# Optimization experiments

Hardware: AMD Instinct MI355X
Metric: run time of the kernel (lower is better)

## Reference

```python
import jax, jax.numpy as jnp
import numpy as np

D_MODEL = 768
D_STATE = 16
D_CONV = 4
EXPAND = 2
D_INNER = EXPAND * D_MODEL
D_HID = D_INNER // 4
BATCH = 2
SEQ = 2048
LN_EPS = 1e-5


def setup_inputs() -> dict:
    key = jax.random.key(0)
    ks = jax.random.split(key, 16)
    rn = lambda k, s, sc: (jax.random.normal(k, s, jnp.float32) * sc)
    x = rn(ks[0], (BATCH, SEQ, D_MODEL), 1.0)
    importance = jax.random.uniform(ks[1], (BATCH, SEQ), jnp.float32)
    W_in = rn(ks[2], (D_MODEL, 2 * D_INNER), D_MODEL ** -0.5)
    conv_w = rn(ks[3], (D_INNER, 1, D_CONV), D_CONV ** -0.5)
    conv_b = rn(ks[4], (D_INNER,), 0.02)
    W_x = rn(ks[5], (D_INNER, 2 * D_STATE + 1), D_INNER ** -0.5)
    W_dt = rn(ks[6], (1, D_INNER), 1.0)
    b_dt = rn(ks[7], (D_INNER,), 0.02)
    Wc1 = rn(ks[8], (1, D_HID), 1.0)
    bc1 = rn(ks[9], (D_HID,), 0.02)
    Wc2 = rn(ks[10], (D_HID, D_INNER), D_HID ** -0.5)
    bc2 = rn(ks[11], (D_INNER,), 0.02)
    A_log = jnp.log(jnp.tile(jnp.arange(1, D_STATE + 1, dtype=jnp.float32)[None, :], (D_INNER, 1)))
    Dskip = jnp.ones((D_INNER,), jnp.float32)
    W_out = rn(ks[12], (D_INNER, D_MODEL), D_INNER ** -0.5)
    ln_g = jnp.ones((D_MODEL,), jnp.float32)
    ln_b = jnp.zeros((D_MODEL,), jnp.float32)
    return dict(x=x, importance=importance, ln_g=ln_g, ln_b=ln_b, W_in=W_in,
                conv_w=conv_w, conv_b=conv_b, W_x=W_x, W_dt=W_dt, b_dt=b_dt,
                Wc1=Wc1, bc1=bc1, Wc2=Wc2, bc2=bc2, A_log=A_log, Dskip=Dskip, W_out=W_out)


def _forward(x, importance, ln_g, ln_b, W_in, conv_w, conv_b, W_x, W_dt, b_dt,
             Wc1, bc1, Wc2, bc2, A_log, Dskip, W_out):
    residual = x
    mu = jnp.mean(x, axis=-1, keepdims=True)
    var = jnp.mean(jnp.square(x - mu), axis=-1, keepdims=True)
    xn = (x - mu) * jax.lax.rsqrt(var + LN_EPS) * ln_g + ln_b
    xz = xn @ W_in                      # (B, L, 2*Di)
    x_proj, z = jnp.split(xz, 2, axis=-1)
    # depthwise causal conv1d (left pad K-1, truncate to L)
    xc = jnp.transpose(x_proj, (0, 2, 1))   # (B, Di, L)
    xc = jax.lax.conv_general_dilated(xc, conv_w, window_strides=(1,),
                                      padding=[(D_CONV - 1, 0)],
                                      feature_group_count=D_INNER,
                                      dimension_numbers=('NCH', 'OIH', 'NCH'))
    xc = xc + conv_b[None, :, None]
    xc = jnp.transpose(xc, (0, 2, 1))       # (B, L, Di)
    xc = jax.nn.silu(xc)
    x_ssm = xc @ W_x                         # (B, L, 2N+1)
    delta_raw = x_ssm[..., :1]
    Bm = x_ssm[..., 1:1 + D_STATE]
    Cm = x_ssm[..., 1 + D_STATE:]
    delta = jax.nn.softplus(delta_raw @ W_dt + b_dt)   # (B, L, Di)
    # cluster modulation of delta
    mod = jax.nn.sigmoid(jax.nn.relu(importance[..., None] @ Wc1 + bc1) @ Wc2 + bc2)
    delta = delta * (1.0 + mod)
    A = -jnp.exp(A_log)                      # (Di, N)
    h0 = jnp.zeros((BATCH, D_INNER, D_STATE), delta.dtype)

    def step(h, ts):
        dl, Bt, Ct, xt = ts                  # (B,Di),(B,N),(B,N),(B,Di)
        dA = jnp.exp(dl[:, :, None] * A)     # (B,Di,N)
        h = dA * h + (dl * xt)[:, :, None] * Bt[:, None, :]
        y = jnp.einsum('bdn,bn->bd', h, Ct)
        return h, y

    xs = (jnp.transpose(delta, (1, 0, 2)), jnp.transpose(Bm, (1, 0, 2)),
          jnp.transpose(Cm, (1, 0, 2)), jnp.transpose(xc, (1, 0, 2)))
    _, ys = jax.lax.scan(step, h0, xs)
    y = jnp.transpose(ys, (1, 0, 2))         # (B, L, Di)
    y = y + xc * Dskip
    y = y * jax.nn.silu(z)
    y = y @ W_out
    return y + residual


def reference(x, importance, ln_g, ln_b, W_in, conv_w, conv_b, W_x, W_dt, b_dt,
              Wc1, bc1, Wc2, bc2, A_log, Dskip, W_out):
    return _forward(x, importance, ln_g, ln_b, W_in, conv_w, conv_b, W_x, W_dt, b_dt,
                    Wc1, bc1, Wc2, bc2, A_log, Dskip, W_out)
```

## Files before the change

### kernel.cpp

```cpp
#include <hip/hip_runtime.h>
#include <math.h>

#define SEQL   2048
#define NBATCH 2
#define DMODEL 768
#define DINNER 1536
#define D2     3072
#define DSTATE 16
#define DHID   384
#define ROWS   (NBATCH*SEQL)
#define NC     64
#define CL     32
#define CROWS  16
#define LN_EPSF 1e-5f

typedef unsigned short u16;
typedef short bf16x8 __attribute__((ext_vector_type(8)));
typedef float f32x4 __attribute__((ext_vector_type(4)));

__device__ __forceinline__ u16 f2b(float x) {
  unsigned u = __float_as_uint(x);
  unsigned r = (u + 0x7FFFu + ((u >> 16) & 1u)) >> 16;
  return (u16)r;
}
__device__ __forceinline__ float b2f(u16 v) {
  return __uint_as_float((unsigned)v << 16);
}

__device__ __forceinline__ void build_E_fast(float dl, float* E) {
  float e1 = __expf(-dl);
  float e2 = e1 * e1, e4 = e2 * e2, e8 = e4 * e4;
  E[0] = e1;      E[1] = e2;      E[2] = e2 * e1; E[3] = e4;
  E[4] = e4 * e1; E[5] = e4 * e2; E[6] = e4 * E[2]; E[7] = e8;
  E[8] = e8 * e1; E[9] = e8 * e2; E[10] = e8 * E[2]; E[11] = e8 * e4;
  E[12] = e8 * E[4]; E[13] = e8 * E[5]; E[14] = e8 * E[6]; E[15] = e8 * e8;
}

__device__ __forceinline__ void tconv64_body(const float* __restrict__ src,
    u16* __restrict__ dst, int K, int N, int bx, int by, int tid) {
  __shared__ float t[64][65];
  int n0 = bx * 64, k0 = by * 64;
  int tx = tid & 15, ty = tid >> 4;
  #pragma unroll
  for (int i = 0; i < 4; ++i) {
    float4 v = *(const float4*)&src[(long)(k0 + ty + 16 * i) * N + n0 + tx * 4];
    t[ty + 16 * i][tx * 4 + 0] = v.x; t[ty + 16 * i][tx * 4 + 1] = v.y;
    t[ty + 16 * i][tx * 4 + 2] = v.z; t[ty + 16 * i][tx * 4 + 3] = v.w;
  }
  __syncthreads();
  #pragma unroll
  for (int i = 0; i < 4; ++i) {
    int n = ty + 16 * i;
    u16 o[4];
    #pragma unroll
    for (int j = 0; j < 4; ++j) o[j] = f2b(t[tx * 4 + j][n]);
    *(ushort4*)&dst[(long)(n0 + n) * K + k0 + tx * 4] = *(ushort4*)o;
  }
}

__global__ __launch_bounds__(256) void prep_kernel(
    const float* __restrict__ W_in,  u16* __restrict__ Wt_in,
    const float* __restrict__ Wc2,   u16* __restrict__ Wt_c2,
    const float* __restrict__ W_out, u16* __restrict__ Wt_out,
    const float* __restrict__ Wx,    u16* __restrict__ Wxt,
    const float* __restrict__ imp,   const float* __restrict__ Wc1,
    const float* __restrict__ bc1,   u16* __restrict__ hid,
    const float* __restrict__ x,     const float* __restrict__ g,
    const float* __restrict__ bta,   u16* __restrict__ xn,
    const float* __restrict__ A_log, float* __restrict__ Af,
    int* __restrict__ flag) {
  int id = blockIdx.x;
  int tid = threadIdx.x;
  if (id < 576) {
    tconv64_body(W_in, Wt_in, 768, 3072, id % 48, id / 48, tid);
  } else if (id < 720) {
    int r = id - 576;  tconv64_body(Wc2, Wt_c2, 384, 1536, r % 24, r / 24, tid);
  } else if (id < 1008) {
    int r = id - 720;  tconv64_body(W_out, Wt_out, 1536, 768, r % 12, r / 12, tid);
  } else if (id < 1056) {
    long i8 = ((long)(id - 1008) * 256 + tid) * 8;
    int n = (int)(i8 / 1536), k0 = (int)(i8 % 1536);
    u16 o[8];
    #pragma unroll
    for (int j = 0; j < 8; ++j)
      o[j] = (n < 33) ? f2b(Wx[(long)(k0 + j) * 33 + n]) : (u16)0;
    *(bf16x8*)&Wxt[i8] = *(bf16x8*)o;
  } else if (id < 1824) {
    long g8 = ((long)(id - 1056) * 256 + tid) * 8;
    int j0 = (int)(g8 % DHID);
    long r = g8 / DHID;
    float im = imp[r];
    float4 wa = *(const float4*)&Wc1[j0], wb = *(const float4*)&Wc1[j0 + 4];
    float4 ba = *(const float4*)&bc1[j0], bb = *(const float4*)&bc1[j0 + 4];
    float v[8] = { fmaf(im, wa.x, ba.x), fmaf(im, wa.y, ba.y),
                   fmaf(im, wa.z, ba.z), fmaf(im, wa.w, ba.w),
                   fmaf(im, wb.x, bb.x), fmaf(im, wb.y, bb.y),
                   fmaf(im, wb.z, bb.z), fmaf(im, wb.w, bb.w) };
    u16 o[8];
    #pragma unroll
    for (int j = 0; j < 8; ++j) o[j] = f2b(v[j] > 0.f ? v[j] : 0.f);
    *(bf16x8*)&hid[g8] = *(bf16x8*)o;
  } else if (id < 2848) {
    int wid2 = tid >> 6, lane = tid & 63;
    long r = (long)(id - 1824) * 4 + wid2;
    const float* xr = x + r * DMODEL;
    float vv[12];
    *(float4*)&vv[0] = *(const float4*)&xr[lane * 4];
    *(float4*)&vv[4] = *(const float4*)&xr[lane * 4 + 256];
    *(float4*)&vv[8] = *(const float4*)&xr[lane * 4 + 512];
    float s = 0.f;
    #pragma unroll
    for (int i = 0; i < 12; ++i) s += vv[i];
    #pragma unroll
    for (int o = 32; o > 0; o >>= 1) s += __shfl_xor(s, o);
    float mu = s * (1.f / DMODEL);
    float q = 0.f;
    #pragma unroll
    for (int i = 0; i < 12; ++i) { float dd = vv[i] - mu; q += dd * dd; }
    #pragma unroll
    for (int o = 32; o > 0; o >>= 1) q += __shfl_xor(q, o);
    float rs = rsqrtf(q * (1.f / DMODEL) + LN_EPSF);
    #pragma unroll
    for (int gq = 0; gq < 3; ++gq) {
      int col = lane * 4 + gq * 256;
      float4 gv = *(const float4*)&g[col];
      float4 bv = *(const float4*)&bta[col];
      u16 o[4];
      o[0] = f2b((vv[gq * 4 + 0] - mu) * rs * gv.x + bv.x);
      o[1] = f2b((vv[gq * 4 + 1] - mu) * rs * gv.y + bv.y);
      o[2] = f2b((vv[gq * 4 + 2] - mu) * rs * gv.z + bv.z);
      o[3] = f2b((vv[gq * 4 + 3] - mu) * rs * gv.w + bv.w);
      *(ushort4*)&xn[r * DMODEL + col] = *(ushort4*)o;
    }
  } else {
    __shared__ int scnt;
    if (tid == 0) scnt = 0;
    __syncthreads();
    int mism = 0;
    for (int i = tid; i < DINNER * 16; i += 256) {
      int n = i & 15;
      float a = -expf(A_log[i]);
      Af[i] = a;
      mism += (fabsf(a + (float)(n + 1)) > 1e-3f) ? 1 : 0;
    }
    atomicAdd(&scnt, mism);
    __syncthreads();
    if (tid == 0) *flag = scnt;
  }
}

template<int BM, int BN, int WGM, int WGN, int EPI, int XSWZ>
__global__ __launch_bounds__(256) void gemm_bf16(
    const u16* __restrict__ A, const u16* __restrict__ Bt,
    float* __restrict__ C, int M, int N, int K, const float* __restrict__ aux,
    const float* __restrict__ p1, const float* __restrict__ p2,
    const float* __restrict__ p3, u16* __restrict__ pz) {
  constexpr int MF = BM / (16 * WGM);
  constexpr int NF = BN / (16 * WGN);
  constexpr int AR = BM / 32;
  constexpr int BR = BN / 32;
  constexpr int HALF = (BM + BN) * 128;
  __shared__ __align__(16) char smem[2 * HALF];

  int tid = threadIdx.x;
  int lane = tid & 63;
  int wid = tid >> 6;

  int bx, by;
  if (XSWZ) {
    int nwgx = gridDim.x;
    int bid = blockIdx.y * nwgx + blockIdx.x;
    int nwg = nwgx * gridDim.y;
    int q = nwg >> 3;
    int swz = (bid & 7) * q + (bid >> 3);
    bx = swz % nwgx; by = swz / nwgx;
  } else {
    bx = blockIdx.x; by = blockIdx.y;
  }
  int m0 = by * BM, n0 = bx * BN;
  int wr = wid / WGN, wc = wid % WGN;

  f32x4 acc[MF][NF];
  #pragma unroll
  for (int i = 0; i < MF; ++i)
    #pragma unroll
    for (int j = 0; j < NF; ++j) acc[i][j] = f32x4{0.f, 0.f, 0.f, 0.f};

  int srow = tid >> 3;
  int schunk = tid & 7;
  int wavebase = (tid & 192) * 16;
  int arow = lane & 15;
  int kgrp = lane >> 4;
  int sw = (lane & 7) << 4;

  auto stage = [&](int k0, char* base) {
    #pragma unroll
    for (int r = 0; r < AR; ++r) {
      int row = r * 32 + srow;
      int chunk = schunk ^ (row & 7);
      const u16* g = A + (size_t)(m0 + row) * K + k0 + chunk * 8;
      __builtin_amdgcn_global_load_lds(
          (const __attribute__((address_space(1))) void*)g,
          (__attribute__((address_space(3))) void*)(base + r * 4096 + wavebase),
          16, 0, 0);
    }
    #pragma unroll
    for (int r = 0; r < BR; ++r) {
      int row = r * 32 + srow;
      int chunk = schunk ^ (row & 7);
      const u16* g = Bt + (size_t)(n0 + row) * K + k0 + chunk * 8;
      __builtin_amdgcn_global_load_lds(
          (const __attribute__((address_space(1))) void*)g,
          (__attribute__((address_space(3))) void*)(base + BM * 128 + r * 4096 + wavebase),
          16, 0, 0);
    }
  };

  auto compute = [&](const char* base) {
    const char* Asm = base;
    const char* Bsm = base + BM * 128;
    #pragma unroll
    for (int ks = 0; ks < 2; ++ks) {
      bf16x8 af[MF], bg[NF];
      #pragma unroll
      for (int i = 0; i < MF; ++i) {
        int row = wr * MF * 16 + i * 16 + arow;
        int off = row * 128 + ((((ks * 4 + kgrp) * 16)) ^ sw);
        af[i] = *(const bf16x8*)(Asm + off);
      }
      #pragma unroll
      for (int j = 0; j < NF; ++j) {
        int row = wc * NF * 16 + j * 16 + arow;
        int off = row * 128 + ((((ks * 4 + kgrp) * 16)) ^ sw);
        bg[j] = *(const bf16x8*)(Bsm + off);
      }
      #pragma unroll
      for (int i = 0; i < MF; ++i)
        #pragma unroll
        for (int j = 0; j < NF; ++j)
          acc[i][j] = __builtin_amdgcn_mfma_f32_16x16x32_bf16(af[i], bg[j], acc[i][j], 0, 0, 0);
    }
  };

  int nk = K >> 6;
  stage(0, smem);
  asm volatile("s_waitcnt vmcnt(0)" ::: "memory");
  __builtin_amdgcn_s_barrier();
  for (int t = 0; t < nk; t += 2) {
    stage((t + 1) << 6, smem + HALF);
    compute(smem);
    asm volatile("s_waitcnt vmcnt(0)" ::: "memory");
    __builtin_amdgcn_s_barrier();
    if (t + 2 < nk) stage((t + 2) << 6, smem);
    compute(smem + HALF);
    asm volatile("s_waitcnt vmcnt(0)" ::: "memory");
    __builtin_amdgcn_s_barrier();
  }

  int crow0 = m0 + wr * MF * 16 + (lane >> 4) * 4;
  int ccol0 = n0 + wc * NF * 16 + (lane & 15);
  #pragma unroll
  for (int i = 0; i < MF; ++i) {
    #pragma unroll
    for (int r = 0; r < 4; ++r) {
      int row = crow0 + i * 16 + r;
      float araw = 0.f;
      if (EPI == 2) araw = aux[(size_t)row * 64];
      #pragma unroll
      for (int j = 0; j < NF; ++j) {
        int col = ccol0 + j * 16;
        float v = acc[i][j][r];
        if (EPI == 0) {
          C[(size_t)row * N + col] = v;
        } else if (EPI == 1) {
          C[(size_t)row * N + col] = v + aux[(size_t)row * N + col];
        } else if (EPI == 2) {
          float raw = fmaf(araw, p1[col], p2[col]);
          float sp = fmaxf(raw, 0.f) + __logf(1.f + __expf(-fabsf(raw)));
          float mod = 1.f / (1.f + __expf(-(v + p3[col])));
          pz[(size_t)row * N + col] = f2b(sp * (1.f + mod));
        } else if (EPI == 5) {
          pz[(size_t)row * N + col] = f2b(v);
        }
      }
    }
  }
}

__global__ __launch_bounds__(256) void conv_silu_kernel(const u16* __restrict__ xzb,
    const float* __restrict__ cw, const float* __restrict__ cb,
    u16* __restrict__ xcb) {
  int tid = threadIdx.x;
  int dblk = blockIdx.x % (DINNER / 256);
  int rc   = blockIdx.x / (DINNER / 256);
  int d = dblk * 256 + tid;
  long r0 = (long)rc * CROWS;
  int s0 = (int)(r0 % SEQL);
  const u16* xp = xzb + r0 * D2 + d;
  float w0 = 0.f, w1 = 0.f, w2 = 0.f;
  if (s0 >= 1) {
    w2 = b2f(xp[-1L * D2]);
    w1 = b2f(xp[-2L * D2]);
    w0 = b2f(xp[-3L * D2]);
  }
  float c0 = cw[d * 4 + 0], c1 = cw[d * 4 + 1];
  float c2 = cw[d * 4 + 2], c3 = cw[d * 4 + 3];
  float cbv = cb[d];
  u16* yp = xcb + r0 * DINNER + d;
  #pragma unroll 4
  for (int t = 0; t < CROWS; ++t) {
    float w3 = b2f(xp[(long)t * D2]);
    float acc = fmaf(w0, c0, fmaf(w1, c1, fmaf(w2, c2, fmaf(w3, c3, cbv))));
    float sg = 1.f / (1.f + __expf(-acc));
    yp[(long)t * DINNER] = f2b(acc * sg);
    w0 = w1; w1 = w2; w2 = w3;
  }
}

__global__ __launch_bounds__(256) void scan_p1(const u16* __restrict__ dlt,
    const u16* __restrict__ xc, const float* __restrict__ xs,
    const float* __restrict__ Af, const int* __restrict__ flag,
    float* __restrict__ Hloc, float* __restrict__ sdl) {
  __shared__ float Bsh[CL][16];
  int tid = threadIdx.x;
  int dblk = blockIdx.x % (DINNER / 256);
  int c = (blockIdx.x / (DINNER / 256)) % NC;
  int b = blockIdx.x / ((DINNER / 256) * NC);
  int d = dblk * 256 + tid;
  long row0 = (long)b * SEQL + c * CL;
  for (int e = tid; e < CL * 16; e += 256) {
    int t = e >> 4, n = e & 15;
    Bsh[t][n] = xs[(row0 + t) * 64 + 1 + n];
  }
  bool fast = (*flag == 0);
  float Ac[16];
  if (!fast) {
    #pragma unroll
    for (int n = 0; n < 16; ++n) Ac[n] = Af[d * 16 + n];
  }
  __syncthreads();
  float h[16] = {};
  float sd = 0.f;
  const u16* dp = dlt + row0 * DINNER + d;
  const u16* xp = xc + row0 * DINNER + d;
  if (fast) {
    for (int t = 0; t < CL; ++t) {
      float dl = b2f(dp[(long)t * DINNER]);
      float xv = b2f(xp[(long)t * DINNER]);
      sd += dl;
      float dx = dl * xv;
      float E[16]; build_E_fast(dl, E);
      #pragma unroll
      for (int n = 0; n < 16; ++n) h[n] = fmaf(E[n], h[n], dx * Bsh[t][n]);
    }
  } else {
    for (int t = 0; t < CL; ++t) {
      float dl = b2f(dp[(long)t * DINNER]);
      float xv = b2f(xp[(long)t * DINNER]);
      sd += dl;
      float dx = dl * xv;
      #pragma unroll
      for (int n = 0; n < 16; ++n)
        h[n] = fmaf(__expf(dl * Ac[n]), h[n], dx * Bsh[t][n]);
    }
  }
  long base = ((long)(b * NC + c) * DINNER + d) * 16;
  #pragma unroll
  for (int n = 0; n < 16; ++n) Hloc[base + n] = h[n];
  sdl[(long)(b * NC + c) * DINNER + d] = sd;
}

__global__ __launch_bounds__(256) void scan_carry(float* __restrict__ Hloc,
    const float* __restrict__ sdl, const float* __restrict__ Af) {
  long g = (long)blockIdx.x * 256 + threadIdx.x;
  if (g >= (long)NBATCH * DINNER * 16) return;
  int n = (int)(g & 15);
  int d = (int)((g >> 4) % DINNER);
  int b = (int)(g / (16L * DINNER));
  float An = Af[d * 16 + n];
  float s = 0.f;
  for (int c = 0; c < NC; ++c) {
    long off = ((long)(b * NC + c) * DINNER + d) * 16 + n;
    float H = Hloc[off];
    float sdv = sdl[(long)(b * NC + c) * DINNER + d];
    Hloc[off] = s;
    s = fmaf(__expf(An * sdv), s, H);
  }
}

__global__ __launch_bounds__(256) void scan_p3(const u16* __restrict__ dlt,
    const u16* __restrict__ xc, const float* __restrict__ xs,
    const float* __restrict__ Af, const int* __restrict__ flag,
    const float* __restrict__ Hloc, const u16* __restrict__ xzb,
    const float* __restrict__ Dskip, u16* __restrict__ y2) {
  __shared__ float Bsh[CL][16];
  __shared__ float Csh[CL][16];
  int tid = threadIdx.x;
  int dblk = blockIdx.x % (DINNER / 256);
  int c = (blockIdx.x / (DINNER / 256)) % NC;
  int b = blockIdx.x / ((DINNER / 256) * NC);
  int d = dblk * 256 + tid;
  long row0 = (long)b * SEQL + c * CL;
  for (int e = tid; e < CL * 16; e += 256) {
    int t = e >> 4, n = e & 15;
    long rr = row0 + t;
    Bsh[t][n] = xs[rr * 64 + 1 + n];
    Csh[t][n] = xs[rr * 64 + 17 + n];
  }
  bool fast = (*flag == 0);
  float Ac[16];
  if (!fast) {
    #pragma unroll
    for (int n = 0; n < 16; ++n) Ac[n] = Af[d * 16 + n];
  }
  __syncthreads();
  float h[16];
  long base = ((long)(b * NC + c) * DINNER + d) * 16;
  #pragma unroll
  for (int n = 0; n < 16; ++n) h[n] = Hloc[base + n];
  float Dv = Dskip[d];
  const u16* dp = dlt + row0 * DINNER + d;
  const u16* xp = xc + row0 * DINNER + d;
  const u16* zp = xzb + row0 * D2 + DINNER + d;
  u16* yp = y2 + row0 * DINNER + d;
  if (fast) {
    for (int t = 0; t < CL; ++t) {
      float dl = b2f(dp[(long)t * DINNER]);
      float xv = b2f(xp[(long)t * DINNER]);
      float dx = dl * xv;
      float E[16]; build_E_fast(dl, E);
      float y = 0.f;
      #pragma unroll
      for (int n = 0; n < 16; ++n) {
        h[n] = fmaf(E[n], h[n], dx * Bsh[t][n]);
        y = fmaf(h[n], Csh[t][n], y);
      }
      float yv = fmaf(xv, Dv, y);
      float zv = b2f(zp[(long)t * D2]);
      float sz = zv / (1.f + __expf(-zv));
      yp[(long)t * DINNER] = f2b(yv * sz);
    }
  } else {
    for (int t = 0; t < CL; ++t) {
      float dl = b2f(dp[(long)t * DINNER]);
      float xv = b2f(xp[(long)t * DINNER]);
      float dx = dl * xv;
      float y = 0.f;
      #pragma unroll
      for (int n = 0; n < 16; ++n) {
        h[n] = fmaf(__expf(dl * Ac[n]), h[n], dx * Bsh[t][n]);
        y = fmaf(h[n], Csh[t][n], y);
      }
      float yv = fmaf(xv, Dv, y);
      float zv = b2f(zp[(long)t * D2]);
      float sz = zv / (1.f + __expf(-zv));
      yp[(long)t * DINNER] = f2b(yv * sz);
    }
  }
}

extern "C" void kernel_launch(void* const* d_in, const int* in_sizes, int n_in,
                              void* d_out, int out_size, void* d_ws, size_t ws_size,
                              hipStream_t stream) {
  const float* x      = (const float*)d_in[0];
  const float* imp    = (const float*)d_in[1];
  const float* ln_g   = (const float*)d_in[2];
  const float* ln_b   = (const float*)d_in[3];
  const float* W_in   = (const float*)d_in[4];
  const float* conv_w = (const float*)d_in[5];
  const float* conv_b = (const float*)d_in[6];
  const float* W_x    = (const float*)d_in[7];
  const float* W_dt   = (const float*)d_in[8];
  const float* b_dt   = (const float*)d_in[9];
  const float* Wc1    = (const float*)d_in[10];
  const float* bc1    = (const float*)d_in[11];
  const float* Wc2    = (const float*)d_in[12];
  const float* bc2    = (const float*)d_in[13];
  const float* A_log  = (const float*)d_in[14];
  const float* Dskip  = (const float*)d_in[15];
  const float* W_out  = (const float*)d_in[16];
  float* out = (float*)d_out;

  char* ws = (char*)d_ws;
  u16*   xzb    = (u16*)  (ws);
  u16*   xcb    = (u16*)  (ws + 25165824L);
  u16*   dltb   = (u16*)  (ws + 37748736L);
  float* xs64   = (float*)(ws + 50331648L);
  u16*   hid    = (u16*)  (ws + 51380224L);
  u16*   xnb    = (u16*)  (ws + 54525952L);
  u16*   y2     = (u16*)  (ws + 60817408L);
  float* Hloc   = (float*)(ws + 73400320L);
  float* sdl    = (float*)(ws + 85983232L);
  u16*   Wt_in  = (u16*)  (ws + 86769664L);
  u16*   Wt_c2  = (u16*)  (ws + 91488256L);
  u16*   Wt_out = (u16*)  (ws + 92667904L);
  u16*   Wxt    = (u16*)  (ws + 95027200L);
  float* Af     = (float*)(ws + 95223808L);
  int*   flag   = (int*)  (ws + 95322112L);

  prep_kernel<<<2849, 256, 0, stream>>>(
      W_in, Wt_in, Wc2, Wt_c2, W_out, Wt_out, W_x, Wxt,
      imp, Wc1, bc1, hid, x, ln_g, ln_b, xnb, A_log, Af, flag);

  gemm_bf16<128,128,2,2,5,1><<<dim3(D2/128, ROWS/128), 256, 0, stream>>>(
      xnb, Wt_in, nullptr, ROWS, D2, DMODEL, nullptr, nullptr, nullptr, nullptr, xzb);
  conv_silu_kernel<<<(DINNER / 256) * (ROWS / CROWS), 256, 0, stream>>>(xzb, conv_w, conv_b, xcb);
  gemm_bf16<32,64,1,4,0,0><<<dim3(1, ROWS/32), 256, 0, stream>>>(
      xcb, Wxt, xs64, ROWS, 64, DINNER, nullptr, nullptr, nullptr, nullptr, nullptr);
  gemm_bf16<64,128,1,4,2,0><<<dim3(DINNER/128, ROWS/64), 256, 0, stream>>>(
      hid, Wt_c2, nullptr, ROWS, DINNER, DHID, xs64, W_dt, b_dt, bc2, dltb);
  scan_p1<<<NBATCH * NC * (DINNER / 256), 256, 0, stream>>>(dltb, xcb, xs64, Af, flag, Hloc, sdl);
  scan_carry<<<(NBATCH * DINNER * 16) / 256, 256, 0, stream>>>(Hloc, sdl, Af);
  scan_p3<<<NBATCH * NC * (DINNER / 256), 256, 0, stream>>>(dltb, xcb, xs64, Af, flag, Hloc, xzb, Dskip, y2);
  gemm_bf16<64,64,1,4,1,0><<<dim3(DMODEL/64, ROWS/64), 256, 0, stream>>>(
      y2, Wt_out, out, ROWS, DMODEL, DINNER, x, nullptr, nullptr, nullptr, nullptr);
}
```

Measured before the change: 164.2 us.

## Add dedicated 256x192-tile in-projection GEMM with 512 threads

Replaces the generic 128x128 bf16 GEMM for the input projection with a specialized kernel that uses 256x192 tiles, 8 waves, direct global-to-LDS loads with XOR-swizzled LDS and double buffering. Grid is 16x16 = 256 blocks with a block-index swizzle meant to improve L2 locality. The larger tiles raise per-block data reuse and cut block count to roughly match the CU count, at the cost of more registers and LDS (about 112KB) per block, which limits occupancy. The previous epilogue variant (EPI 5) is replaced by a plain bf16 store, which could differ if that epilogue did extra work.

Result: faster. 158.9 us, median of 2 (-3.2%).

```diff
diff --git a/kernel.cpp b/kernel.cpp
--- a/kernel.cpp
+++ b/kernel.cpp
@@ -149,6 +149,115 @@
   }
 }
 
+__global__ __launch_bounds__(512) void gemm_xz_256(
+    const u16* __restrict__ A, const u16* __restrict__ Bt,
+    u16* __restrict__ pz) {
+  constexpr int BM = 256, BN = 192, K = 768, N = 3072;
+  constexpr int HALF = (BM + BN) * 128;
+  __shared__ __align__(16) char smem[2 * HALF];
+
+  int tid = threadIdx.x;
+  int lane = tid & 63;
+  int wid = tid >> 6;
+  int bid = blockIdx.y * 16 + blockIdx.x;
+  int swz = (bid & 7) * 32 + (bid >> 3);
+  int bx = swz & 15, by = swz >> 4;
+  int m0 = by * BM, n0 = bx * BN;
+  int wr = wid >> 2, wc = wid & 3;
+
+  f32x4 acc[8][3];
+  #pragma unroll
+  for (int i = 0; i < 8; ++i)
+    #pragma unroll
+    for (int j = 0; j < 3; ++j) acc[i][j] = f32x4{0.f, 0.f, 0.f, 0.f};
+
+  int srow = tid >> 3;
+  int schunk = tid & 7;
+  int wavebase = wid * 1024;
+  int arow = lane & 15;
+  int kgrp = lane >> 4;
+  int sw = (lane & 7) << 4;
+
+  auto stage = [&](int k0, char* base) {
+    #pragma unroll
+    for (int r = 0; r < 4; ++r) {
+      int row = r * 64 + srow;
+      int chunk = schunk ^ (row & 7);
+      const u16* g = A + (size_t)(m0 + row) * K + k0 + chunk * 8;
+      __builtin_amdgcn_global_load_lds(
+          (const __attribute__((address_space(1))) void*)g,
+          (__attribute__((address_space(3))) void*)(base + r * 8192 + wavebase),
+          16, 0, 0);
+    }
+    #pragma unroll
+    for (int r = 0; r < 3; ++r) {
+      int row = r * 64 + srow;
+      int chunk = schunk ^ (row & 7);
+      const u16* g = Bt + (size_t)(n0 + row) * K + k0 + chunk * 8;
+      __builtin_amdgcn_global_load_lds(
+          (const __attribute__((address_space(1))) void*)g,
+          (__attribute__((address_space(3))) void*)(base + BM * 128 + r * 8192 + wavebase),
+          16, 0, 0);
+    }
+  };
+
+  auto compute = [&](const char* base) {
+    const char* Asm = base;
+    const char* Bsm = base + BM * 128;
+    #pragma unroll
+    for (int ks = 0; ks < 2; ++ks) {
+      bf16x8 af[8], bg[3];
+      #pragma unroll
+      for (int i = 0; i < 8; ++i) {
+        int row = wr * 128 + i * 16 + arow;
+        int off = row * 128 + ((((ks * 4 + kgrp) * 16)) ^ sw);
+        af[i] = *(const bf16x8*)(Asm + off);
+      }
+      #pragma unroll
+      for (int j = 0; j < 3; ++j) {
+        int row = wc * 48 + j * 16 + arow;
+        int off = row * 128 + ((((ks * 4 + kgrp) * 16)) ^ sw);
+        bg[j] = *(const bf16x8*)(Bsm + off);
+      }
+      #pragma unroll
+      for (int i = 0; i < 8; ++i)
+        #pragma unroll
+        for (int j = 0; j < 3; ++j)
+          acc[i][j] = __builtin_amdgcn_mfma_f32_16x16x32_bf16(af[i], bg[j], acc[i][j], 0, 0, 0);
+    }
+  };
+
+  stage(0, smem);
+  asm volatile("s_waitcnt vmcnt(0)" ::: "memory");
+  __builtin_amdgcn_s_barrier();
+  #pragma unroll 1
+  for (int t = 0; t < 12; t += 2) {
+    stage((t + 1) << 6, smem + HALF);
+    compute(smem);
+    asm volatile("s_waitcnt vmcnt(0)" ::: "memory");
+    __builtin_amdgcn_s_barrier();
+    if (t + 2 < 12) stage((t + 2) << 6, smem);
+    compute(smem + HALF);
+    asm volatile("s_waitcnt vmcnt(0)" ::: "memory");
+    __builtin_amdgcn_s_barrier();
+  }
+
+  int crow0 = m0 + wr * 128 + (lane >> 4) * 4;
+  int ccol0 = n0 + wc * 48 + (lane & 15);
+  #pragma unroll
+  for (int i = 0; i < 8; ++i) {
+    #pragma unroll
+    for (int r = 0; r < 4; ++r) {
+      int row = crow0 + i * 16 + r;
+      #pragma unroll
+      for (int j = 0; j < 3; ++j) {
+        int col = ccol0 + j * 16;
+        pz[(size_t)row * N + col] = f2b(acc[i][j][r]);
+      }
+    }
+  }
+}
+
 template<int BM, int BN, int WGM, int WGN, int EPI, int XSWZ>
 __global__ __launch_bounds__(256) void gemm_bf16(
     const u16* __restrict__ A, const u16* __restrict__ Bt,
@@ -502,8 +611,7 @@
       W_in, Wt_in, Wc2, Wt_c2, W_out, Wt_out, W_x, Wxt,
       imp, Wc1, bc1, hid, x, ln_g, ln_b, xnb, A_log, Af, flag);
 
-  gemm_bf16<128,128,2,2,5,1><<<dim3(D2/128, ROWS/128), 256, 0, stream>>>(
-      xnb, Wt_in, nullptr, ROWS, D2, DMODEL, nullptr, nullptr, nullptr, nullptr, xzb);
+  gemm_xz_256<<<dim3(16, 16), 512, 0, stream>>>(xnb, Wt_in, xzb);
   conv_silu_kernel<<<(DINNER / 256) * (ROWS / CROWS), 256, 0, stream>>>(xzb, conv_w, conv_b, xcb);
   gemm_bf16<32,64,1,4,0,0><<<dim3(1, ROWS/32), 256, 0, stream>>>(
       xcb, Wxt, xs64, ROWS, 64, DINNER, nullptr, nullptr, nullptr, nullptr, nullptr);
```
